# Performance work log

Measured on AMD Instinct MI355X. Metric: run time of the kernel, lower is better.

Reference implementation:

```python
import jax, jax.numpy as jnp
import numpy as np

B, S, D = 4, 2048, 1024
H, HD = 16, 64  # n_head, head_dim; H*HD == D

def setup_inputs() -> dict:
    key = jax.random.key(0)
    k1, k2, k3 = jax.random.split(key, 3)
    x = jax.random.normal(k1, (B, S, D), dtype=jnp.float32)
    # nn.Linear weights: stored [out, in]; init ~ U(-1/sqrt(in), 1/sqrt(in))
    w_attn = jax.random.uniform(k2, (3 * D, D), dtype=jnp.float32,
                                minval=-1.0, maxval=1.0) / jnp.sqrt(jnp.float32(D))
    w_proj = jax.random.uniform(k3, (D, D), dtype=jnp.float32,
                                minval=-1.0, maxval=1.0) / jnp.sqrt(jnp.float32(D))
    return {"x": x, "w_attn": w_attn, "w_proj": w_proj}

def reference(x, w_attn, w_proj):
    b, s, d = x.shape
    qkv = jnp.einsum('bsd,ed->bse', x, w_attn)              # [b, s, 3D]
    q, k, v = jnp.split(qkv, 3, axis=-1)
    q = q.reshape(b, s, H, HD).transpose(0, 2, 1, 3)        # [b, h, s, hd]
    k = k.reshape(b, s, H, HD).transpose(0, 2, 1, 3)
    v = v.reshape(b, s, H, HD).transpose(0, 2, 1, 3)
    scale = 1.0 / jnp.sqrt(jnp.float32(HD))
    scores = jnp.einsum('bhqd,bhkd->bhqk', q, k) * scale    # [b, h, s, s]
    causal = jnp.tril(jnp.ones((s, s), dtype=bool))
    scores = jnp.where(causal[None, None], scores, -jnp.inf)
    attn = jax.nn.softmax(scores, axis=-1)
    out = jnp.einsum('bhqk,bhkd->bhqd', attn, v)            # [b, h, s, hd]
    out = out.transpose(0, 2, 1, 3).reshape(b, s, d)
    return jnp.einsum('bsd,ed->bse', out, w_proj)
```

## Files before the change

### kernel.cpp

```cpp
#include <hip/hip_runtime.h>
#include <hip/hip_bf16.h>

#define NB   4
#define SEQ  2048
#define DMODEL 1024
#define NHEAD 16
#define HDIM 64
#define MROWS (NB * SEQ)
#define N_QKV (3 * DMODEL)

typedef __attribute__((ext_vector_type(8))) short bf16x8;
typedef __attribute__((ext_vector_type(4))) float f32x4;
typedef __attribute__((ext_vector_type(2))) unsigned int u32x2;

#define MFMA16(a, b, c) __builtin_amdgcn_mfma_f32_16x16x32_bf16((a), (b), (c), 0, 0, 0)

__device__ inline bf16x8 load16(const __hip_bfloat16* p) {
    union { uint4 u; bf16x8 v; } t;
    t.u = *(const uint4*)p;
    return t.v;
}

__device__ inline ushort f2bf(float f) {
    union { float f; unsigned int u; } a;
    a.f = f;
    unsigned int r = a.u + 0x7FFFu + ((a.u >> 16) & 1u);
    return (ushort)(r >> 16);
}

__device__ inline unsigned int cvt_pk_bf16(float lo, float hi) {
    unsigned int r;
    asm("v_cvt_pk_bf16_f32 %0, %1, %2" : "=v"(r) : "v"(lo), "v"(hi));
    return r;
}

__device__ inline void gload_lds16(const __hip_bfloat16* g, __hip_bfloat16* l) {
    __builtin_amdgcn_global_load_lds(
        (const __attribute__((address_space(1))) unsigned int*)g,
        (__attribute__((address_space(3))) unsigned int*)l,
        16, 0, 0);
}

__global__ __launch_bounds__(256)
void cast3_kernel(const float* __restrict__ x, const float* __restrict__ wa,
                  const float* __restrict__ wp, ushort* __restrict__ xb,
                  ushort* __restrict__ wab, ushort* __restrict__ wpb, float qsc) {
    const int bid = (int)blockIdx.x;
    const float* in; ushort* out; int idx; float s = 1.0f;
    if (bid < 8192) {
        in = x;  out = xb;  idx = (bid * 256 + (int)threadIdx.x) * 4;
    } else if (bid < 11264) {
        in = wa; out = wab; idx = ((bid - 8192) * 256 + (int)threadIdx.x) * 4;
        if (idx < DMODEL * DMODEL) s = qsc;
    } else {
        in = wp; out = wpb; idx = ((bid - 11264) * 256 + (int)threadIdx.x) * 4;
    }
    float4 v = *(const float4*)(in + idx);
    ushort4 o;
    o.x = f2bf(v.x * s);
    o.y = f2bf(v.y * s);
    o.z = f2bf(v.z * s);
    o.w = f2bf(v.w * s);
    *(ushort4*)(out + idx) = o;
}

template<int MODE>
__global__ __launch_bounds__(512, 4)
void gemm_bt(const __hip_bfloat16* __restrict__ A,
             const __hip_bfloat16* __restrict__ Bm,
             ushort* __restrict__ Cb,
             float* __restrict__ Cf,
             ushort* __restrict__ Vt,
             int M, int N, int K) {
    constexpr int BM = 256, BN = 128, BK = 32;
    __shared__ __hip_bfloat16 As[3 * BM * BK];
    __shared__ __hip_bfloat16 Bs[3 * BN * BK];

    const int tid  = threadIdx.x;
    const int wave = tid >> 6;
    const int lane = tid & 63;
    const int quad = lane >> 4;
    const int l16  = lane & 15;
    const int wr = (wave >> 1) * 64;
    const int wc = (wave & 1) * 64;

    const int nbx  = gridDim.x;
    const int nblk = nbx * gridDim.y;
    const int orig = (int)blockIdx.y * nbx + (int)blockIdx.x;
    const int swzb = (orig & 7) * (nblk >> 3) + (orig >> 3);
    const int bx = swzb % nbx, by = swzb / nbx;

    const int row0 = by * BM;
    const int col0 = bx * BN;

    const int srow = tid >> 2;
    const int ssl  = ((tid & 3) ^ ((tid >> 3) & 3)) * 8;
    const __hip_bfloat16* ag0 = A  + (size_t)(row0 +       srow) * K + ssl;
    const __hip_bfloat16* ag1 = A  + (size_t)(row0 + 128 + srow) * K + ssl;
    const __hip_bfloat16* bg0 = Bm + (size_t)(col0 +       srow) * K + ssl;

    auto stage = [&](int buf) {
        gload_lds16(ag0, As + buf * (BM * BK) + wave * 512);
        gload_lds16(ag1, As + buf * (BM * BK) + 4096 + wave * 512);
        gload_lds16(bg0, Bs + buf * (BN * BK) + wave * 512);
        ag0 += BK; ag1 += BK; bg0 += BK;
    };

    f32x4 acc[4][4];
#pragma unroll
    for (int i = 0; i < 4; i++)
#pragma unroll
        for (int j = 0; j < 4; j++) acc[i][j] = (f32x4)0.0f;

    stage(0);
    stage(1);
    asm volatile("s_waitcnt vmcnt(3)" ::: "memory");
    __builtin_amdgcn_s_barrier();
    asm volatile("" ::: "memory");

    const int nk = K / BK;
    const int swzr = (l16 >> 1) & 3;
    for (int t = 0; t < nk; ++t) {
        const int cur = t % 3;
        const bool more = (t + 2 < nk);
        if (more) stage((t + 2) % 3);

        const __hip_bfloat16* Ab = As + cur * (BM * BK);
        const __hip_bfloat16* Bb = Bs + cur * (BN * BK);
        bf16x8 af[4], bfr[4];
#pragma unroll
        for (int i = 0; i < 4; i++) {
            af[i]  = load16(&Ab[(wr + i * 16 + l16) * 32 + ((quad ^ swzr) * 8)]);
            bfr[i] = load16(&Bb[(wc + i * 16 + l16) * 32 + ((quad ^ swzr) * 8)]);
        }

        __builtin_amdgcn_s_setprio(1);
#pragma unroll
        for (int i = 0; i < 4; i++)
#pragma unroll
            for (int j = 0; j < 4; j++)
                acc[i][j] = MFMA16(af[i], bfr[j], acc[i][j]);
        __builtin_amdgcn_s_setprio(0);

        if (more) asm volatile("s_waitcnt vmcnt(3)" ::: "memory");
        else      asm volatile("s_waitcnt vmcnt(0)" ::: "memory");
        __builtin_amdgcn_s_barrier();
        asm volatile("" ::: "memory");
    }

    if constexpr (MODE == 2) {
        if (col0 >= 2 * DMODEL) {
            const int vcol0 = col0 - 2 * DMODEL;
            const int bb = row0 >> 11;
            const int row0m = row0 & 2047;
            const int hh = (vcol0 >> 6) + (wave & 1);
            ushort* Tw = (ushort*)As + wave * 2048;
            ushort* vdst = Vt + ((size_t)(bb * NHEAD + hh) * HDIM) * SEQ;
#pragma unroll
            for (int P = 0; P < 2; P++) {
#pragma unroll
                for (int i2 = 0; i2 < 2; i2++)
#pragma unroll
                    for (int j = 0; j < 4; j++)
#pragma unroll
                        for (int r = 0; r < 4; r++)
                            Tw[(j * 16 + l16) * 32 + i2 * 16 + quad * 4 + r] =
                                f2bf(acc[2 * P + i2][j][r]);
#pragma unroll
                for (int pp = 0; pp < 4; pp++) {
                    int d = pp * 16 + (lane >> 2);
                    int part = lane & 3;
                    uint4 v = *(const uint4*)(Tw + d * 32 + part * 8);
                    *(uint4*)(vdst + (size_t)d * SEQ + row0m + wr + P * 32 + part * 8) = v;
                }
            }
            return;
        }
    }

    ushort* base = nullptr;
    int c0 = 0;
    if constexpr (MODE == 2) {
        base = Cb + ((col0 >= DMODEL) ? (size_t)MROWS * DMODEL : 0);
        c0 = col0 & (DMODEL - 1);
    }
#pragma unroll
    for (int i = 0; i < 4; i++) {
#pragma unroll
        for (int r = 0; r < 4; r++) {
            size_t grow = (size_t)(row0 + wr + i * 16 + quad * 4 + r);
#pragma unroll
            for (int j = 0; j < 4; j++) {
                float v = acc[i][j][r];
                if (MODE == 1) {
                    Cf[grow * N + col0 + wc + j * 16 + l16] = v;
                } else {
                    base[grow * DMODEL + c0 + wc + j * 16 + l16] = f2bf(v);
                }
            }
        }
    }
}

__global__ __launch_bounds__(256)
void attn_kernel(const ushort* __restrict__ Qb, const ushort* __restrict__ Kb,
                 const ushort* __restrict__ Vtb, ushort* __restrict__ O) {
    __shared__ __hip_bfloat16 Kc[4 * 32 * 64];
    __shared__ __hip_bfloat16 Vc[4 * 64 * 32];

    const int tid  = threadIdx.x;
    const int wave = tid >> 6;
    const int lane = tid & 63;
    const int quad = lane >> 4;
    const int l16  = lane & 15;

    const int blk = (int)blockIdx.x;
    const int g   = 15 - (blk >> 6);
    const int bh  = (((blk >> 3) & 7) << 3) | (blk & 7);
    const int b = bh >> 4, h = bh & 15;
    const int p  = 4 * g + wave;
    const int q0 = p * 32;
    const int nc = p + 1;
    const int ncmax = 4 * g + 4;

    bf16x8 ones;
#pragma unroll
    for (int i = 0; i < 8; i++) ones[i] = (short)0x3F80;
    const f32x4 fzero = (f32x4)0.0f;

    bf16x8 qf[2][2];
#pragma unroll
    for (int s = 0; s < 2; s++) {
        const __hip_bfloat16* qp = (const __hip_bfloat16*)Qb
            + ((size_t)b * SEQ + q0 + s * 16 + l16) * DMODEL + h * HDIM;
        qf[s][0] = load16(qp + quad * 8);
        qf[s][1] = load16(qp + 32 + quad * 8);
    }

    const __hip_bfloat16* kbase = (const __hip_bfloat16*)Kb + (size_t)b * SEQ * DMODEL + h * HDIM;
    const __hip_bfloat16* vbase = (const __hip_bfloat16*)Vtb + (size_t)bh * HDIM * SEQ;

    f32x4 oacc[2][4], lacc[2];
#pragma unroll
    for (int s = 0; s < 2; s++) {
        lacc[s] = (f32x4)0.0f;
#pragma unroll
        for (int t = 0; t < 4; t++) oacc[s][t] = (f32x4)0.0f;
    }

    const int slot = wave * 64 + lane;
    const int skey = slot >> 3;
    const int sdsg = (slot & 7) ^ (skey & 7);
    const int svd  = slot >> 2;
    const int svsg = (slot & 3) ^ ((svd >> 1) & 3);
    const __hip_bfloat16* kg = kbase + (size_t)skey * DMODEL + sdsg * 8;
    const __hip_bfloat16* vg = vbase + (size_t)svd * SEQ + svsg * 8;

    auto stage = [&](int buf, int chunk) {
        gload_lds16(kg + (size_t)chunk * (32 * DMODEL), Kc + buf * 2048 + wave * 512);
        gload_lds16(vg + (size_t)chunk * 32,            Vc + buf * 2048 + wave * 512);
    };

    stage(0, 0);
    stage(1, 1);
    asm volatile("s_waitcnt vmcnt(2)" ::: "memory");
    __builtin_amdgcn_s_barrier();
    asm volatile("" ::: "memory");

    const int vswz = (l16 >> 1) & 3;

    for (int cb = 0; cb < ncmax; cb += 4) {
#pragma unroll
        for (int u = 0; u < 4; ++u) {
            const int c = cb + u;
            const bool more = (c + 2 < ncmax);
            if (more) stage((u + 2) & 3, c + 2);

            if (c < nc) {
                const int k0 = c * 32;
                const bool diag = (c == nc - 1);
                const __hip_bfloat16* Kb_l = Kc + u * 2048;
                const __hip_bfloat16* Vb_l = Vc + u * 2048;

                bf16x8 kb[2][2], vb[4];
#pragma unroll
                for (int t = 0; t < 2; t++) {
#pragma unroll
                    for (int hf = 0; hf < 2; hf++)
                        kb[t][hf] = load16(&Kb_l[(t * 16 + l16) * 64
                                                 + (((hf * 4 + quad) ^ (l16 & 7)) * 8)]);
                }
#pragma unroll
                for (int t = 0; t < 4; t++)
                    vb[t] = load16(&Vb_l[(t * 16 + l16) * 32 + ((quad ^ vswz) * 8)]);

#pragma unroll
                for (int s = 0; s < 2; s++) {
                    f32x4 z[2];
#pragma unroll
                    for (int t = 0; t < 2; t++) {
                        f32x4 zz = MFMA16(kb[t][0], qf[s][0], fzero);
                        zz = MFMA16(kb[t][1], qf[s][1], zz);
                        z[t] = zz;
                    }

                    unsigned int xw0, xw1, yw0, yw1;
#pragma unroll
                    for (int t = 0; t < 2; t++) {
                        float e[4];
#pragma unroll
                        for (int r = 0; r < 4; r++) {
                            float sv = z[t][r];
                            if (diag) {
                                int key = k0 + t * 16 + quad * 4 + r;
                                int qq  = q0 + s * 16 + l16;
                                sv = (key <= qq) ? sv : -1e30f;
                            }
                            e[r] = __builtin_amdgcn_exp2f(sv);
                        }
                        unsigned int w0 = cvt_pk_bf16(e[0], e[1]);
                        unsigned int w1 = cvt_pk_bf16(e[2], e[3]);
                        if (t == 0) { xw0 = w0; xw1 = w1; }
                        else        { yw0 = w0; yw1 = w1; }
                    }

                    u32x2 s32_0 = __builtin_amdgcn_permlane32_swap(xw0, yw0, false, false);
                    u32x2 fin_0 = __builtin_amdgcn_permlane16_swap(s32_0.x, s32_0.y, false, false);
                    u32x2 s32_1 = __builtin_amdgcn_permlane32_swap(xw1, yw1, false, false);
                    u32x2 fin_1 = __builtin_amdgcn_permlane16_swap(s32_1.x, s32_1.y, false, false);
                    union { unsigned int u[4]; bf16x8 v; } pk;
                    pk.u[0] = fin_0.x; pk.u[1] = fin_1.x;
                    pk.u[2] = fin_0.y; pk.u[3] = fin_1.y;
                    bf16x8 pa = pk.v;

#pragma unroll
                    for (int t = 0; t < 4; t++)
                        oacc[s][t] = MFMA16(pa, vb[t], oacc[s][t]);
                    lacc[s] = MFMA16(pa, ones, lacc[s]);
                }
            }

            if (more) asm volatile("s_waitcnt vmcnt(2)" ::: "memory");
            else      asm volatile("s_waitcnt vmcnt(0)" ::: "memory");
            __builtin_amdgcn_s_barrier();
            asm volatile("" ::: "memory");
        }
    }

#pragma unroll
    for (int s = 0; s < 2; s++) {
        float inv[4];
#pragma unroll
        for (int r = 0; r < 4; r++) inv[r] = 1.0f / lacc[s][r];
#pragma unroll
        for (int t = 0; t < 4; t++) {
#pragma unroll
            for (int r = 0; r < 4; r++) {
                float v = oacc[s][t][r] * inv[r];
                O[((size_t)b * SEQ + q0 + s * 16 + quad * 4 + r) * DMODEL
                  + h * HDIM + t * 16 + l16] = f2bf(v);
            }
        }
    }
}

extern "C" void kernel_launch(void* const* d_in, const int* in_sizes, int n_in,
                              void* d_out, int out_size, void* d_ws, size_t ws_size,
                              hipStream_t stream) {
    const float* x      = (const float*)d_in[0];
    const float* w_attn = (const float*)d_in[1];
    const float* w_proj = (const float*)d_in[2];
    float* out = (float*)d_out;

    ushort* ws   = (ushort*)d_ws;
    ushort* xb   = ws;
    ushort* wab  = xb  + (size_t)MROWS * DMODEL;
    ushort* wpb  = wab + (size_t)N_QKV * DMODEL;
    ushort* qkvb = wpb + (size_t)DMODEL * DMODEL;
    ushort* ob   = qkvb + (size_t)MROWS * N_QKV;

    ushort* qreg = qkvb;
    ushort* kreg = qkvb + (size_t)MROWS * DMODEL;
    ushort* vtreg = qkvb + 2 * (size_t)MROWS * DMODEL;

    const float qsc = 0.125f * 1.44269504f;

    cast3_kernel<<<12288, 256, 0, stream>>>(x, w_attn, w_proj, xb, wab, wpb, qsc);

    gemm_bt<2><<<dim3(N_QKV / 128, MROWS / 256), 512, 0, stream>>>(
        (const __hip_bfloat16*)xb, (const __hip_bfloat16*)wab, qreg, nullptr, vtreg,
        MROWS, N_QKV, DMODEL);

    attn_kernel<<<1024, 256, 0, stream>>>(qreg, kreg, vtreg, ob);

    gemm_bt<1><<<dim3(DMODEL / 128, MROWS / 256), 512, 0, stream>>>(
        (const __hip_bfloat16*)ob, (const __hip_bfloat16*)wpb, nullptr, out, nullptr,
        MROWS, DMODEL, DMODEL);
}
```

Before: 239.1 us.

## Use 4-wave GEMM blocks with 64x128 per-wave tiles

The GEMM kernels now run with 256 threads (4 waves) instead of 512, and each wave computes a 64x128 output tile (4x8 MFMA accumulators) rather than 64x64. This raises operand reuse from registers per LDS load and cuts the number of LDS fragment reads per MFMA. In exchange it doubles accumulator register pressure and halves waves per block, which may lower occupancy and latency hiding. The V-transpose epilogue is reworked to match, and now packs pairs of bf16 values into 32-bit LDS stores.

```diff
diff --git a/kernel.cpp b/kernel.cpp
--- a/kernel.cpp
+++ b/kernel.cpp
@@ -65,7 +65,7 @@
 }
 
 template<int MODE>
-__global__ __launch_bounds__(512, 4)
+__global__ __launch_bounds__(256, 2)
 void gemm_bt(const __hip_bfloat16* __restrict__ A,
              const __hip_bfloat16* __restrict__ Bm,
              ushort* __restrict__ Cb,
@@ -81,8 +81,7 @@
     const int lane = tid & 63;
     const int quad = lane >> 4;
     const int l16  = lane & 15;
-    const int wr = (wave >> 1) * 64;
-    const int wc = (wave & 1) * 64;
+    const int wr = wave * 64;
 
     const int nbx  = gridDim.x;
     const int nblk = nbx * gridDim.y;
@@ -95,26 +94,30 @@
 
     const int srow = tid >> 2;
     const int ssl  = ((tid & 3) ^ ((tid >> 3) & 3)) * 8;
-    const __hip_bfloat16* ag0 = A  + (size_t)(row0 +       srow) * K + ssl;
-    const __hip_bfloat16* ag1 = A  + (size_t)(row0 + 128 + srow) * K + ssl;
-    const __hip_bfloat16* bg0 = Bm + (size_t)(col0 +       srow) * K + ssl;
+    const __hip_bfloat16* ag = A  + (size_t)(row0 + srow) * K + ssl;
+    const __hip_bfloat16* bg = Bm + (size_t)(col0 + srow) * K + ssl;
 
     auto stage = [&](int buf) {
-        gload_lds16(ag0, As + buf * (BM * BK) + wave * 512);
-        gload_lds16(ag1, As + buf * (BM * BK) + 4096 + wave * 512);
-        gload_lds16(bg0, Bs + buf * (BN * BK) + wave * 512);
-        ag0 += BK; ag1 += BK; bg0 += BK;
+#pragma unroll
+        for (int q = 0; q < 4; q++)
+            gload_lds16(ag + (size_t)(q * 64) * K,
+                        As + buf * 8192 + q * 2048 + wave * 512);
+#pragma unroll
+        for (int q = 0; q < 2; q++)
+            gload_lds16(bg + (size_t)(q * 64) * K,
+                        Bs + buf * 4096 + q * 2048 + wave * 512);
+        ag += BK; bg += BK;
     };
 
-    f32x4 acc[4][4];
+    f32x4 acc[4][8];
 #pragma unroll
     for (int i = 0; i < 4; i++)
 #pragma unroll
-        for (int j = 0; j < 4; j++) acc[i][j] = (f32x4)0.0f;
+        for (int j = 0; j < 8; j++) acc[i][j] = (f32x4)0.0f;
 
     stage(0);
     stage(1);
-    asm volatile("s_waitcnt vmcnt(3)" ::: "memory");
+    asm volatile("s_waitcnt vmcnt(6)" ::: "memory");
     __builtin_amdgcn_s_barrier();
     asm volatile("" ::: "memory");
 
@@ -125,24 +128,25 @@
         const bool more = (t + 2 < nk);
         if (more) stage((t + 2) % 3);
 
-        const __hip_bfloat16* Ab = As + cur * (BM * BK);
-        const __hip_bfloat16* Bb = Bs + cur * (BN * BK);
-        bf16x8 af[4], bfr[4];
-#pragma unroll
-        for (int i = 0; i < 4; i++) {
+        const __hip_bfloat16* Ab = As + cur * 8192;
+        const __hip_bfloat16* Bb = Bs + cur * 4096;
+        bf16x8 af[4], bfr[8];
+#pragma unroll
+        for (int i = 0; i < 4; i++)
             af[i]  = load16(&Ab[(wr + i * 16 + l16) * 32 + ((quad ^ swzr) * 8)]);
-            bfr[i] = load16(&Bb[(wc + i * 16 + l16) * 32 + ((quad ^ swzr) * 8)]);
-        }
+#pragma unroll
+        for (int j = 0; j < 8; j++)
+            bfr[j] = load16(&Bb[(j * 16 + l16) * 32 + ((quad ^ swzr) * 8)]);
 
         __builtin_amdgcn_s_setprio(1);
 #pragma unroll
         for (int i = 0; i < 4; i++)
 #pragma unroll
-            for (int j = 0; j < 4; j++)
+            for (int j = 0; j < 8; j++)
                 acc[i][j] = MFMA16(af[i], bfr[j], acc[i][j]);
         __builtin_amdgcn_s_setprio(0);
 
-        if (more) asm volatile("s_waitcnt vmcnt(3)" ::: "memory");
+        if (more) asm volatile("s_waitcnt vmcnt(6)" ::: "memory");
         else      asm volatile("s_waitcnt vmcnt(0)" ::: "memory");
         __builtin_amdgcn_s_barrier();
         asm volatile("" ::: "memory");
@@ -153,25 +157,34 @@
             const int vcol0 = col0 - 2 * DMODEL;
             const int bb = row0 >> 11;
             const int row0m = row0 & 2047;
-            const int hh = (vcol0 >> 6) + (wave & 1);
-            ushort* Tw = (ushort*)As + wave * 2048;
-            ushort* vdst = Vt + ((size_t)(bb * NHEAD + hh) * HDIM) * SEQ;
-#pragma unroll
-            for (int P = 0; P < 2; P++) {
-#pragma unroll
-                for (int i2 = 0; i2 < 2; i2++)
-#pragma unroll
-                    for (int j = 0; j < 4; j++)
-#pragma unroll
-                        for (int r = 0; r < 4; r++)
-                            Tw[(j * 16 + l16) * 32 + i2 * 16 + quad * 4 + r] =
-                                f2bf(acc[2 * P + i2][j][r]);
-#pragma unroll
-                for (int pp = 0; pp < 4; pp++) {
-                    int d = pp * 16 + (lane >> 2);
-                    int part = lane & 3;
-                    uint4 v = *(const uint4*)(Tw + d * 32 + part * 8);
-                    *(uint4*)(vdst + (size_t)d * SEQ + row0m + wr + P * 32 + part * 8) = v;
+            ushort* Tw0 = (ushort*)As + wave * 4096;
+#pragma unroll
+            for (int hh2 = 0; hh2 < 2; hh2++) {
+                const int hh = (vcol0 >> 6) + hh2;
+                ushort* vdst = Vt + ((size_t)(bb * NHEAD + hh) * HDIM) * SEQ;
+#pragma unroll
+                for (int P = 0; P < 2; P++) {
+                    ushort* Tw = Tw0 + ((hh2 * 2 + P) & 1) * 2048;
+#pragma unroll
+                    for (int i2 = 0; i2 < 2; i2++)
+#pragma unroll
+                        for (int j = 0; j < 4; j++) {
+                            const f32x4 a = acc[2 * P + i2][hh2 * 4 + j];
+                            const int d = j * 16 + l16;
+                            unsigned int w0 = (unsigned int)f2bf(a[0])
+                                            | ((unsigned int)f2bf(a[1]) << 16);
+                            unsigned int w1 = (unsigned int)f2bf(a[2])
+                                            | ((unsigned int)f2bf(a[3]) << 16);
+                            *(unsigned int*)&Tw[d * 32 + i2 * 16 + quad * 4]     = w0;
+                            *(unsigned int*)&Tw[d * 32 + i2 * 16 + quad * 4 + 2] = w1;
+                        }
+#pragma unroll
+                    for (int pp = 0; pp < 4; pp++) {
+                        int d = pp * 16 + (lane >> 2);
+                        int part = lane & 3;
+                        uint4 v = *(const uint4*)(Tw + d * 32 + part * 8);
+                        *(uint4*)(vdst + (size_t)d * SEQ + row0m + wr + P * 32 + part * 8) = v;
+                    }
                 }
             }
             return;
@@ -190,12 +203,12 @@
         for (int r = 0; r < 4; r++) {
             size_t grow = (size_t)(row0 + wr + i * 16 + quad * 4 + r);
 #pragma unroll
-            for (int j = 0; j < 4; j++) {
+            for (int j = 0; j < 8; j++) {
                 float v = acc[i][j][r];
                 if (MODE == 1) {
-                    Cf[grow * N + col0 + wc + j * 16 + l16] = v;
+                    Cf[grow * N + col0 + j * 16 + l16] = v;
                 } else {
-                    base[grow * DMODEL + c0 + wc + j * 16 + l16] = f2bf(v);
+                    base[grow * DMODEL + c0 + j * 16 + l16] = f2bf(v);
                 }
             }
         }
@@ -387,13 +400,13 @@
 
     cast3_kernel<<<12288, 256, 0, stream>>>(x, w_attn, w_proj, xb, wab, wpb, qsc);
 
-    gemm_bt<2><<<dim3(N_QKV / 128, MROWS / 256), 512, 0, stream>>>(
+    gemm_bt<2><<<dim3(N_QKV / 128, MROWS / 256), 256, 0, stream>>>(
         (const __hip_bfloat16*)xb, (const __hip_bfloat16*)wab, qreg, nullptr, vtreg,
         MROWS, N_QKV, DMODEL);
 
     attn_kernel<<<1024, 256, 0, stream>>>(qreg, kreg, vtreg, ob);
 
-    gemm_bt<1><<<dim3(DMODEL / 128, MROWS / 256), 512, 0, stream>>>(
+    gemm_bt<1><<<dim3(DMODEL / 128, MROWS / 256), 256, 0, stream>>>(
         (const __hip_bfloat16*)ob, (const __hip_bfloat16*)wpb, nullptr, out, nullptr,
         MROWS, DMODEL, DMODEL);
 }
```

Result: slower. 255.2 us (+6.8%).

## Double GEMM K-tile depth and split each step into interleaved load/MFMA phases

Applied to the files above, without the earlier changes.

The bf16 GEMM k-tile grows from 32 to 64, with a new 8-way XOR LDS swizzle, and launch bounds drop to 2 blocks per CU because LDS use doubles. Each iteration is now split into two halves: LDS fragment reads and global-to-LDS prefetches for tile t+2 are interleaved with MFMA groups, separated by extra barriers. The aim is fewer loop iterations and barriers per unit of K, and better overlap of memory with MFMA work. The cost is lower occupancy, more barriers per iteration and higher register pressure.

```diff
diff --git a/kernel.cpp b/kernel.cpp
--- a/kernel.cpp
+++ b/kernel.cpp
@@ -65,14 +65,14 @@
 }
 
 template<int MODE>
-__global__ __launch_bounds__(512, 4)
+__global__ __launch_bounds__(512, 2)
 void gemm_bt(const __hip_bfloat16* __restrict__ A,
              const __hip_bfloat16* __restrict__ Bm,
              ushort* __restrict__ Cb,
              float* __restrict__ Cf,
              ushort* __restrict__ Vt,
              int M, int N, int K) {
-    constexpr int BM = 256, BN = 128, BK = 32;
+    constexpr int BM = 256, BN = 128, BK = 64;
     __shared__ __hip_bfloat16 As[3 * BM * BK];
     __shared__ __hip_bfloat16 Bs[3 * BN * BK];
 
@@ -83,6 +83,7 @@
     const int l16  = lane & 15;
     const int wr = (wave >> 1) * 64;
     const int wc = (wave & 1) * 64;
+    const int sw8 = l16 & 7;
 
     const int nbx  = gridDim.x;
     const int nblk = nbx * gridDim.y;
@@ -93,18 +94,19 @@
     const int row0 = by * BM;
     const int col0 = bx * BN;
 
-    const int srow = tid >> 2;
-    const int ssl  = ((tid & 3) ^ ((tid >> 3) & 3)) * 8;
-    const __hip_bfloat16* ag0 = A  + (size_t)(row0 +       srow) * K + ssl;
-    const __hip_bfloat16* ag1 = A  + (size_t)(row0 + 128 + srow) * K + ssl;
-    const __hip_bfloat16* bg0 = Bm + (size_t)(col0 +       srow) * K + ssl;
-
-    auto stage = [&](int buf) {
-        gload_lds16(ag0, As + buf * (BM * BK) + wave * 512);
-        gload_lds16(ag1, As + buf * (BM * BK) + 4096 + wave * 512);
-        gload_lds16(bg0, Bs + buf * (BN * BK) + wave * 512);
-        ag0 += BK; ag1 += BK; bg0 += BK;
+    const int srow = tid >> 3;
+    const int ssl  = ((tid & 7) ^ ((tid >> 3) & 7)) * 8;
+    const __hip_bfloat16* ag = A  + (size_t)(row0 + srow) * K + ssl;
+    const __hip_bfloat16* bg = Bm + (size_t)(col0 + srow) * K + ssl;
+
+    auto stageA = [&](int q, int tile, int buf) {
+        gload_lds16(ag + (size_t)tile * BK + (size_t)(q * 64) * K,
+                    As + buf * 16384 + q * 4096 + wave * 512);
     };
+    auto stageB = [&](int q, int tile, int buf) {
+        gload_lds16(bg + (size_t)tile * BK + (size_t)(q * 64) * K,
+                    Bs + buf * 8192 + q * 4096 + wave * 512);
+    };
 
     f32x4 acc[4][4];
 #pragma unroll
@@ -112,40 +114,80 @@
 #pragma unroll
         for (int j = 0; j < 4; j++) acc[i][j] = (f32x4)0.0f;
 
-    stage(0);
-    stage(1);
-    asm volatile("s_waitcnt vmcnt(3)" ::: "memory");
+#pragma unroll
+    for (int q = 0; q < 4; q++) stageA(q, 0, 0);
+    stageB(0, 0, 0); stageB(1, 0, 0);
+#pragma unroll
+    for (int q = 0; q < 4; q++) stageA(q, 1, 1);
+    stageB(0, 1, 1); stageB(1, 1, 1);
+    asm volatile("s_waitcnt vmcnt(6)" ::: "memory");
     __builtin_amdgcn_s_barrier();
     asm volatile("" ::: "memory");
 
     const int nk = K / BK;
-    const int swzr = (l16 >> 1) & 3;
+    int cur = 0;
     for (int t = 0; t < nk; ++t) {
-        const int cur = t % 3;
         const bool more = (t + 2 < nk);
-        if (more) stage((t + 2) % 3);
-
-        const __hip_bfloat16* Ab = As + cur * (BM * BK);
-        const __hip_bfloat16* Bb = Bs + cur * (BN * BK);
-        bf16x8 af[4], bfr[4];
-#pragma unroll
-        for (int i = 0; i < 4; i++) {
-            af[i]  = load16(&Ab[(wr + i * 16 + l16) * 32 + ((quad ^ swzr) * 8)]);
-            bfr[i] = load16(&Bb[(wc + i * 16 + l16) * 32 + ((quad ^ swzr) * 8)]);
-        }
-
+        const int nb = (cur + 2 >= 3) ? cur - 1 : cur + 2;
+        const __hip_bfloat16* Ab = As + cur * 16384;
+        const __hip_bfloat16* Bb = Bs + cur * 8192;
+
+        bf16x8 a0[2][2], bfr[4][2];
+#pragma unroll
+        for (int i2 = 0; i2 < 2; i2++)
+#pragma unroll
+            for (int ks = 0; ks < 2; ks++)
+                a0[i2][ks] = load16(&Ab[(wr + i2 * 16 + l16) * 64
+                                        + (((ks * 4 + quad) ^ sw8) * 8)]);
+#pragma unroll
+        for (int j = 0; j < 4; j++)
+#pragma unroll
+            for (int ks = 0; ks < 2; ks++)
+                bfr[j][ks] = load16(&Bb[(wc + j * 16 + l16) * 64
+                                        + (((ks * 4 + quad) ^ sw8) * 8)]);
+        if (more) { stageA(0, t + 2, nb); stageA(1, t + 2, nb); stageB(0, t + 2, nb); }
+
+        __builtin_amdgcn_s_barrier();
+        asm volatile("" ::: "memory");
         __builtin_amdgcn_s_setprio(1);
 #pragma unroll
-        for (int i = 0; i < 4; i++)
-#pragma unroll
-            for (int j = 0; j < 4; j++)
-                acc[i][j] = MFMA16(af[i], bfr[j], acc[i][j]);
+        for (int i2 = 0; i2 < 2; i2++)
+#pragma unroll
+            for (int j = 0; j < 4; j++) {
+                acc[i2][j] = MFMA16(a0[i2][0], bfr[j][0], acc[i2][j]);
+                acc[i2][j] = MFMA16(a0[i2][1], bfr[j][1], acc[i2][j]);
+            }
         __builtin_amdgcn_s_setprio(0);
-
-        if (more) asm volatile("s_waitcnt vmcnt(3)" ::: "memory");
+        __builtin_amdgcn_s_barrier();
+        asm volatile("" ::: "memory");
+
+        bf16x8 a1[2][2];
+#pragma unroll
+        for (int i2 = 0; i2 < 2; i2++)
+#pragma unroll
+            for (int ks = 0; ks < 2; ks++)
+                a1[i2][ks] = load16(&Ab[(wr + 32 + i2 * 16 + l16) * 64
+                                        + (((ks * 4 + quad) ^ sw8) * 8)]);
+        if (more) { stageA(2, t + 2, nb); stageA(3, t + 2, nb); stageB(1, t + 2, nb); }
+
+        __builtin_amdgcn_s_barrier();
+        asm volatile("" ::: "memory");
+        __builtin_amdgcn_s_setprio(1);
+#pragma unroll
+        for (int i2 = 0; i2 < 2; i2++)
+#pragma unroll
+            for (int j = 0; j < 4; j++) {
+                acc[2 + i2][j] = MFMA16(a1[i2][0], bfr[j][0], acc[2 + i2][j]);
+                acc[2 + i2][j] = MFMA16(a1[i2][1], bfr[j][1], acc[2 + i2][j]);
+            }
+        __builtin_amdgcn_s_setprio(0);
+
+        if (more) asm volatile("s_waitcnt vmcnt(6)" ::: "memory");
         else      asm volatile("s_waitcnt vmcnt(0)" ::: "memory");
         __builtin_amdgcn_s_barrier();
         asm volatile("" ::: "memory");
+
+        cur = (cur == 2) ? 0 : cur + 1;
     }
 
     if constexpr (MODE == 2) {
```

Result: faster. 232.8 us (-2.6%).
